# Kernel optimization log

Hardware: AMD Instinct MI355X
Metric: run time of the kernel (lower is better)

Reference implementation:

```python
import jax, jax.numpy as jnp
import numpy as np

T = 0.2
EPS = 1e-05


def setup_inputs() -> dict:
    key = jax.random.key(0)
    k1, k2 = jax.random.split(key)
    N, D, NUM_CLASSES = 8192, 128, 128
    inp = jax.random.normal(k1, (N, D), dtype=jnp.float32)
    label = jax.random.randint(k2, (N,), 0, NUM_CLASSES, dtype=jnp.int64)
    return {"input": inp, "label": label}


def reference(input, label):
    # Pairwise cosine similarity: dot(x_i, x_j) / max(||x_i|| * ||x_j||, eps)
    norms = jnp.sqrt(jnp.sum(input * input, axis=1))            # [N]
    denom = jnp.maximum(norms[:, None] * norms[None, :], EPS)   # [N, N]
    sim = (input @ input.T) / denom                             # [N, N]

    mask = (label[:, None] == label[None, :]).astype(input.dtype)  # same-label mask
    e = jnp.exp(sim / T)
    e = e - jnp.diag(jnp.diag(e))                               # zero the diagonal

    pos = mask * e                                              # positives (diag already 0)
    unsim = jnp.sum(e - pos, axis=-1, keepdims=True)            # [N, 1] negatives row-sum
    ratio = pos / (pos + unsim)                                 # per-pair NT-Xent prob
    safe = jnp.where(ratio > 0, ratio, 1.0)                     # loss[loss<=0] = 1
    loss_sum = jnp.sum(-jnp.log(safe))

    # number of off-diagonal positive pairs
    off_diag_mask = mask - jnp.diag(jnp.diag(mask))
    n_pos = jnp.count_nonzero(off_diag_mask).astype(input.dtype)
    return loss_sum / n_pos
```

## Files before the change

kernel.cpp:

```cpp
#include <hip/hip_runtime.h>
#include <math.h>

typedef float f32x4 __attribute__((ext_vector_type(4)));
typedef __attribute__((address_space(3))) unsigned int lds_u32;
typedef __attribute__((address_space(1))) const unsigned int glb_u32;

__global__ __launch_bounds__(256) void norm_kernel(
    const float* __restrict__ X, unsigned char* __restrict__ Y8,
    float inv_sqrtT) {
  int t = threadIdx.x;
  int row = blockIdx.x * 8 + (t >> 5);
  int l32 = t & 31;
  float4 v = ((const float4*)(X + (size_t)row * 128))[l32];
  float s = v.x * v.x + v.y * v.y + v.z * v.z + v.w * v.w;
  s += __shfl_xor(s, 1);
  s += __shfl_xor(s, 2);
  s += __shfl_xor(s, 4);
  s += __shfl_xor(s, 8);
  s += __shfl_xor(s, 16);
  float inv = inv_sqrtT * rsqrtf(fmaxf(s, 1e-24f));
  int pk = __builtin_amdgcn_cvt_pk_fp8_f32(v.x * inv, v.y * inv, 0, false);
  pk = __builtin_amdgcn_cvt_pk_fp8_f32(v.z * inv, v.w * inv, pk, true);
  int chunk = l32 >> 2;
  int off = ((chunk ^ (row & 7)) << 4) + ((l32 & 3) << 2);
  *(unsigned int*)(Y8 + (size_t)row * 128 + off) = (unsigned)pk;
}

__global__ __launch_bounds__(256, 2) void pass1_kernel(
    const unsigned char* __restrict__ Y8, const int* __restrict__ lab,
    float* __restrict__ P, float* __restrict__ Q, float* __restrict__ S,
    int N) {
  __shared__ unsigned char As[128][128];
  __shared__ unsigned char Bs[2][128][128];
  __shared__ int labR[128];
  __shared__ float tsumS[128], psumS[128], diagS[128];
  __shared__ float sS[4];

  const int b = blockIdx.x;
  const int bi = b >> 3, c = b & 7;
  const int i0 = bi * 128;
  const int t = threadIdx.x;
  const int w = t >> 6, lane = t & 63;

#pragma unroll
  for (int k = 0; k < 4; ++k) {
    const int c0 = w * 64 + k * 256;
    const int cc = c0 + lane;
    __builtin_amdgcn_global_load_lds(
        (glb_u32*)(Y8 + (size_t)i0 * 128 + (size_t)cc * 16),
        (lds_u32*)((unsigned char*)&As[0][0] + c0 * 16), 16, 0, 0);
    __builtin_amdgcn_global_load_lds(
        (glb_u32*)(Y8 + (size_t)(c * 8) * 128 * 128 + (size_t)cc * 16),
        (lds_u32*)((unsigned char*)&Bs[0][0][0] + c0 * 16), 16, 0, 0);
  }
  if (t < 128) {
    labR[t] = lab[i0 + t];
    psumS[t] = 0.f;
    diagS[t] = 0.f;
  }
  __syncthreads();

  const int quad = lane >> 4, l16 = lane & 15;
  const int rbase = w * 32;
  const int sw = l16 & 7;

  long af[4][2];
#pragma unroll
  for (int ks = 0; ks < 4; ++ks) {
    const int ch = ks * 2 + (quad >> 1);
    const int off = ((ch ^ sw) << 4) + ((quad & 1) << 3);
#pragma unroll
    for (int p = 0; p < 2; ++p)
      af[ks][p] = *(const long*)&As[rbase + p * 16 + l16][off];
  }
  int lr[2][4];
#pragma unroll
  for (int pi = 0; pi < 2; ++pi)
#pragma unroll
    for (int r = 0; r < 4; ++r)
      lr[pi][r] = labR[rbase + pi * 16 + quad * 4 + r];

  float trow[2][4] = {};
  float sacc = 0.f;

#pragma unroll 2
  for (int jt = 0; jt < 8; ++jt) {
    const int cur = jt & 1;
    const int jtile = c * 8 + jt;
    const int jt0 = jtile * 128;

    if (jt < 7) {
      const unsigned char* src = Y8 + (size_t)(jt0 + 128) * 128;
      unsigned char* dst = (unsigned char*)&Bs[cur ^ 1][0][0];
#pragma unroll
      for (int k = 0; k < 4; ++k) {
        const int c0 = w * 64 + k * 256;
        const int cc = c0 + lane;
        __builtin_amdgcn_global_load_lds((glb_u32*)(src + (size_t)cc * 16),
                                         (lds_u32*)(dst + c0 * 16), 16, 0, 0);
      }
    }

    int lc[8];
#pragma unroll
    for (int pj = 0; pj < 8; ++pj) lc[pj] = lab[jt0 + pj * 16 + l16];

    f32x4 acc[2][8] = {};
#pragma unroll
    for (int ks = 0; ks < 4; ++ks) {
      const int ch = ks * 2 + (quad >> 1);
      const int off = ((ch ^ sw) << 4) + ((quad & 1) << 3);
      long bf[8];
#pragma unroll
      for (int p = 0; p < 8; ++p)
        bf[p] = *(const long*)&Bs[cur][p * 16 + l16][off];
#pragma unroll
      for (int pi = 0; pi < 2; ++pi)
#pragma unroll
        for (int pj = 0; pj < 8; ++pj)
          acc[pi][pj] = __builtin_amdgcn_mfma_f32_16x16x32_fp8_fp8(
              af[ks][pi], bf[pj], acc[pi][pj], 0, 0, 0);
    }

    const bool dtile = (jtile == bi);
#pragma unroll
    for (int pi = 0; pi < 2; ++pi)
#pragma unroll
      for (int pj = 0; pj < 8; ++pj)
#pragma unroll
        for (int r = 0; r < 4; ++r) {
          const float s = acc[pi][pj][r];
          const float e = __expf(s);
          trow[pi][r] += e;
          if (lr[pi][r] == lc[pj]) {
            const int rowl = rbase + pi * 16 + quad * 4 + r;
            const int cl = pj * 16 + l16;
            if (dtile && rowl == cl) {
              diagS[rowl] = e;
            } else {
              atomicAdd(&psumS[rowl], e);
              sacc += s;
            }
          }
        }
    __syncthreads();
  }

#pragma unroll
  for (int pi = 0; pi < 2; ++pi)
#pragma unroll
    for (int r = 0; r < 4; ++r) {
      float v = trow[pi][r];
      v += __shfl_xor(v, 1);
      v += __shfl_xor(v, 2);
      v += __shfl_xor(v, 4);
      v += __shfl_xor(v, 8);
      if (l16 == 0) tsumS[rbase + pi * 16 + quad * 4 + r] = v;
    }
#pragma unroll
  for (int m = 1; m < 64; m <<= 1) sacc += __shfl_xor(sacc, m);
  if (lane == 0) sS[w] = sacc;
  __syncthreads();

  if (t < 128) {
    const int gi = i0 + t;
    P[c * N + gi] = tsumS[t] - diagS[t];
    Q[c * N + gi] = psumS[t];
  }
  if (t == 0) S[b] = sS[0] + sS[1] + sS[2] + sS[3];
}

__global__ __launch_bounds__(1024) void finalize_kernel(
    const int* __restrict__ lab, const float* __restrict__ P,
    const float* __restrict__ Q, const float* __restrict__ S,
    float* __restrict__ out, int N) {
  __shared__ int hist[256];
  __shared__ float redL[16], redN[16], redS[16];
  int t = threadIdx.x;
  int lane = t & 63, w = t >> 6;
  if (t < 256) hist[t] = 0;
  __syncthreads();
  for (int i = t; i < N; i += 1024) atomicAdd(&hist[lab[i] & 255], 1);
  __syncthreads();
  float local = 0.f;
  for (int i = t; i < N; i += 1024) {
    float tot = 0.f, p = 0.f;
#pragma unroll
    for (int cc = 0; cc < 8; ++cc) {
      tot += P[cc * N + i];
      p += Q[cc * N + i];
    }
    float u = tot - p;
    float cnt = (float)(hist[lab[i] & 255] - 1);
    local += cnt * __logf(u) + p / u;
  }
  float nposl = 0.f;
  if (t < 256) {
    float m = (float)hist[t];
    nposl = m * m;
  }
  float sl = (t < 512) ? S[t] : 0.f;
#pragma unroll
  for (int msk = 1; msk < 64; msk <<= 1) {
    local += __shfl_xor(local, msk);
    nposl += __shfl_xor(nposl, msk);
    sl += __shfl_xor(sl, msk);
  }
  if (lane == 0) {
    redL[w] = local;
    redN[w] = nposl;
    redS[w] = sl;
  }
  __syncthreads();
  if (t == 0) {
    float ls = 0.f, np = 0.f, ss = 0.f;
#pragma unroll
    for (int i = 0; i < 16; ++i) {
      ls += redL[i];
      np += redN[i];
      ss += redS[i];
    }
    out[0] = (ls - ss) / (np - (float)N);
  }
}

extern "C" void kernel_launch(void* const* d_in, const int* in_sizes, int n_in,
                              void* d_out, int out_size, void* d_ws,
                              size_t ws_size, hipStream_t stream) {
  const float* X = (const float*)d_in[0];
  const int* lab = (const int*)d_in[1];
  float* out = (float*)d_out;

  const int N = in_sizes[1];

  unsigned char* Y8 = (unsigned char*)d_ws;
  float* P = (float*)(Y8 + (size_t)N * 128);
  float* Q = P + 8 * (size_t)N;
  float* S = Q + 8 * (size_t)N;

  const float inv_sqrtT = 2.2360679775f;
  norm_kernel<<<N / 8, 256, 0, stream>>>(X, Y8, inv_sqrtT);

  const int nblk = (N / 128) * 8;
  pass1_kernel<<<nblk, 256, 0, stream>>>(Y8, lab, P, Q, S, N);
  finalize_kernel<<<1, 1024, 0, stream>>>(lab, P, Q, S, out, N);
}
```

Before: 98.47 us.

## Split column work finer, drop LDS atomics, parallelize finalize across blocks

The main pass now gives each block a 512-column slice, processed as eight 64-column tiles, with 16 column groups instead of 8. That doubles the grid and halves the B-tile LDS footprint so four blocks can share a CU. The per-row positive sums now accumulate in registers with branchless selects, replacing shared-memory atomics, and diagonal handling only happens in the phase that holds the diagonal. The finalize step is spread over N/256 blocks that atomically add into an output zeroed by the norm kernel. In exchange, A fragments are re-read from LDS every tile, the histogram is rebuilt in every finalize block, and the float atomic sum is no longer deterministic.

```diff
diff --git a/kernel.cpp b/kernel.cpp
--- a/kernel.cpp
+++ b/kernel.cpp
@@ -7,7 +7,7 @@
 
 __global__ __launch_bounds__(256) void norm_kernel(
     const float* __restrict__ X, unsigned char* __restrict__ Y8,
-    float inv_sqrtT) {
+    float* __restrict__ out, float inv_sqrtT) {
   int t = threadIdx.x;
   int row = blockIdx.x * 8 + (t >> 5);
   int l32 = t & 31;
@@ -24,21 +24,22 @@
   int chunk = l32 >> 2;
   int off = ((chunk ^ (row & 7)) << 4) + ((l32 & 3) << 2);
   *(unsigned int*)(Y8 + (size_t)row * 128 + off) = (unsigned)pk;
-}
-
-__global__ __launch_bounds__(256, 2) void pass1_kernel(
+  if (blockIdx.x == 0 && t == 0) out[0] = 0.f;
+}
+
+__global__ __launch_bounds__(256, 4) void pass1_kernel(
     const unsigned char* __restrict__ Y8, const int* __restrict__ lab,
     float* __restrict__ P, float* __restrict__ Q, float* __restrict__ S,
     int N) {
   __shared__ unsigned char As[128][128];
-  __shared__ unsigned char Bs[2][128][128];
+  __shared__ unsigned char Bs[2][64][128];
   __shared__ int labR[128];
-  __shared__ float tsumS[128], psumS[128], diagS[128];
   __shared__ float sS[4];
 
   const int b = blockIdx.x;
-  const int bi = b >> 3, c = b & 7;
+  const int bi = b >> 4, c = b & 15;
   const int i0 = bi * 128;
+  const int j0 = c * 512;
   const int t = threadIdx.x;
   const int w = t >> 6, lane = t & 63;
 
@@ -49,30 +50,22 @@
     __builtin_amdgcn_global_load_lds(
         (glb_u32*)(Y8 + (size_t)i0 * 128 + (size_t)cc * 16),
         (lds_u32*)((unsigned char*)&As[0][0] + c0 * 16), 16, 0, 0);
+  }
+#pragma unroll
+  for (int k = 0; k < 2; ++k) {
+    const int c0 = w * 64 + k * 256;
+    const int cc = c0 + lane;
     __builtin_amdgcn_global_load_lds(
-        (glb_u32*)(Y8 + (size_t)(c * 8) * 128 * 128 + (size_t)cc * 16),
+        (glb_u32*)(Y8 + (size_t)j0 * 128 + (size_t)cc * 16),
         (lds_u32*)((unsigned char*)&Bs[0][0][0] + c0 * 16), 16, 0, 0);
   }
-  if (t < 128) {
-    labR[t] = lab[i0 + t];
-    psumS[t] = 0.f;
-    diagS[t] = 0.f;
-  }
+  if (t < 128) labR[t] = lab[i0 + t];
   __syncthreads();
 
   const int quad = lane >> 4, l16 = lane & 15;
   const int rbase = w * 32;
   const int sw = l16 & 7;
 
-  long af[4][2];
-#pragma unroll
-  for (int ks = 0; ks < 4; ++ks) {
-    const int ch = ks * 2 + (quad >> 1);
-    const int off = ((ch ^ sw) << 4) + ((quad & 1) << 3);
-#pragma unroll
-    for (int p = 0; p < 2; ++p)
-      af[ks][p] = *(const long*)&As[rbase + p * 16 + l16][off];
-  }
   int lr[2][4];
 #pragma unroll
   for (int pi = 0; pi < 2; ++pi)
@@ -81,19 +74,18 @@
       lr[pi][r] = labR[rbase + pi * 16 + quad * 4 + r];
 
   float trow[2][4] = {};
+  float pr[2][4] = {};
   float sacc = 0.f;
 
-#pragma unroll 2
   for (int jt = 0; jt < 8; ++jt) {
     const int cur = jt & 1;
-    const int jtile = c * 8 + jt;
-    const int jt0 = jtile * 128;
+    const int jt0 = j0 + jt * 64;
 
     if (jt < 7) {
-      const unsigned char* src = Y8 + (size_t)(jt0 + 128) * 128;
+      const unsigned char* src = Y8 + (size_t)(jt0 + 64) * 128;
       unsigned char* dst = (unsigned char*)&Bs[cur ^ 1][0][0];
 #pragma unroll
-      for (int k = 0; k < 4; ++k) {
+      for (int k = 0; k < 2; ++k) {
         const int c0 = w * 64 + k * 256;
         const int cc = c0 + lane;
         __builtin_amdgcn_global_load_lds((glb_u32*)(src + (size_t)cc * 16),
@@ -101,48 +93,65 @@
       }
     }
 
-    int lc[8];
-#pragma unroll
-    for (int pj = 0; pj < 8; ++pj) lc[pj] = lab[jt0 + pj * 16 + l16];
-
-    f32x4 acc[2][8] = {};
+    int lc[4], cg[4];
+#pragma unroll
+    for (int pj = 0; pj < 4; ++pj) {
+      cg[pj] = jt0 + pj * 16 + l16;
+      lc[pj] = lab[cg[pj]];
+    }
+
+    f32x4 acc[2][4] = {};
 #pragma unroll
     for (int ks = 0; ks < 4; ++ks) {
       const int ch = ks * 2 + (quad >> 1);
       const int off = ((ch ^ sw) << 4) + ((quad & 1) << 3);
-      long bf[8];
-#pragma unroll
-      for (int p = 0; p < 8; ++p)
+      long af[2], bf[4];
+#pragma unroll
+      for (int p = 0; p < 2; ++p)
+        af[p] = *(const long*)&As[rbase + p * 16 + l16][off];
+#pragma unroll
+      for (int p = 0; p < 4; ++p)
         bf[p] = *(const long*)&Bs[cur][p * 16 + l16][off];
 #pragma unroll
       for (int pi = 0; pi < 2; ++pi)
 #pragma unroll
-        for (int pj = 0; pj < 8; ++pj)
+        for (int pj = 0; pj < 4; ++pj)
           acc[pi][pj] = __builtin_amdgcn_mfma_f32_16x16x32_fp8_fp8(
-              af[ks][pi], bf[pj], acc[pi][pj], 0, 0, 0);
-    }
-
-    const bool dtile = (jtile == bi);
-#pragma unroll
-    for (int pi = 0; pi < 2; ++pi)
-#pragma unroll
-      for (int pj = 0; pj < 8; ++pj)
-#pragma unroll
-        for (int r = 0; r < 4; ++r) {
-          const float s = acc[pi][pj][r];
-          const float e = __expf(s);
-          trow[pi][r] += e;
-          if (lr[pi][r] == lc[pj]) {
+              af[pi], bf[pj], acc[pi][pj], 0, 0, 0);
+    }
+
+    const bool dphase = ((jt0 >> 7) == bi);
+    if (dphase) {
+#pragma unroll
+      for (int pi = 0; pi < 2; ++pi)
+#pragma unroll
+        for (int pj = 0; pj < 4; ++pj)
+#pragma unroll
+          for (int r = 0; r < 4; ++r) {
+            const float s = acc[pi][pj][r];
+            const float e = __expf(s);
             const int rowl = rbase + pi * 16 + quad * 4 + r;
-            const int cl = pj * 16 + l16;
-            if (dtile && rowl == cl) {
-              diagS[rowl] = e;
-            } else {
-              atomicAdd(&psumS[rowl], e);
-              sacc += s;
-            }
+            const bool self = (i0 + rowl) == cg[pj];
+            const bool match = (lr[pi][r] == lc[pj]) && !self;
+            trow[pi][r] += self ? 0.f : e;
+            pr[pi][r] += match ? e : 0.f;
+            sacc += match ? s : 0.f;
           }
-        }
+    } else {
+#pragma unroll
+      for (int pi = 0; pi < 2; ++pi)
+#pragma unroll
+        for (int pj = 0; pj < 4; ++pj)
+#pragma unroll
+          for (int r = 0; r < 4; ++r) {
+            const float s = acc[pi][pj][r];
+            const float e = __expf(s);
+            const bool match = (lr[pi][r] == lc[pj]);
+            trow[pi][r] += e;
+            pr[pi][r] += match ? e : 0.f;
+            sacc += match ? s : 0.f;
+          }
+    }
     __syncthreads();
   }
 
@@ -150,77 +159,63 @@
   for (int pi = 0; pi < 2; ++pi)
 #pragma unroll
     for (int r = 0; r < 4; ++r) {
-      float v = trow[pi][r];
+      float v = trow[pi][r], q = pr[pi][r];
       v += __shfl_xor(v, 1);
+      q += __shfl_xor(q, 1);
       v += __shfl_xor(v, 2);
+      q += __shfl_xor(q, 2);
       v += __shfl_xor(v, 4);
+      q += __shfl_xor(q, 4);
       v += __shfl_xor(v, 8);
-      if (l16 == 0) tsumS[rbase + pi * 16 + quad * 4 + r] = v;
+      q += __shfl_xor(q, 8);
+      if (l16 == 0) {
+        const int row = rbase + pi * 16 + quad * 4 + r;
+        P[c * N + i0 + row] = v;
+        Q[c * N + i0 + row] = q;
+      }
     }
 #pragma unroll
   for (int m = 1; m < 64; m <<= 1) sacc += __shfl_xor(sacc, m);
   if (lane == 0) sS[w] = sacc;
   __syncthreads();
-
-  if (t < 128) {
-    const int gi = i0 + t;
-    P[c * N + gi] = tsumS[t] - diagS[t];
-    Q[c * N + gi] = psumS[t];
-  }
   if (t == 0) S[b] = sS[0] + sS[1] + sS[2] + sS[3];
 }
 
-__global__ __launch_bounds__(1024) void finalize_kernel(
+__global__ __launch_bounds__(256) void finalize_kernel(
     const int* __restrict__ lab, const float* __restrict__ P,
     const float* __restrict__ Q, const float* __restrict__ S,
     float* __restrict__ out, int N) {
   __shared__ int hist[256];
-  __shared__ float redL[16], redN[16], redS[16];
-  int t = threadIdx.x;
-  int lane = t & 63, w = t >> 6;
-  if (t < 256) hist[t] = 0;
-  __syncthreads();
-  for (int i = t; i < N; i += 1024) atomicAdd(&hist[lab[i] & 255], 1);
-  __syncthreads();
-  float local = 0.f;
-  for (int i = t; i < N; i += 1024) {
-    float tot = 0.f, p = 0.f;
-#pragma unroll
-    for (int cc = 0; cc < 8; ++cc) {
-      tot += P[cc * N + i];
-      p += Q[cc * N + i];
-    }
-    float u = tot - p;
-    float cnt = (float)(hist[lab[i] & 255] - 1);
-    local += cnt * __logf(u) + p / u;
-  }
-  float nposl = 0.f;
-  if (t < 256) {
-    float m = (float)hist[t];
-    nposl = m * m;
-  }
-  float sl = (t < 512) ? S[t] : 0.f;
-#pragma unroll
-  for (int msk = 1; msk < 64; msk <<= 1) {
-    local += __shfl_xor(local, msk);
-    nposl += __shfl_xor(nposl, msk);
-    sl += __shfl_xor(sl, msk);
-  }
-  if (lane == 0) {
-    redL[w] = local;
-    redN[w] = nposl;
-    redS[w] = sl;
-  }
+  __shared__ float red[4];
+  const int b = blockIdx.x, t = threadIdx.x;
+  const int lane = t & 63, w = t >> 6;
+  hist[t] = 0;
+  __syncthreads();
+  for (int i = t; i < N; i += 256) atomicAdd(&hist[lab[i] & 255], 1);
+  __syncthreads();
+
+  const int i = b * 256 + t;
+  float tot = 0.f, p = 0.f;
+#pragma unroll
+  for (int cc = 0; cc < 16; ++cc) {
+    tot += P[cc * N + i];
+    p += Q[cc * N + i];
+  }
+  const float u = tot - p;
+  const float cnti = (float)(hist[lab[i] & 255] - 1);
+  float local = cnti * __logf(u) + p / u;
+  if (t < 32) local -= S[b * 32 + t];
+#pragma unroll
+  for (int m = 1; m < 64; m <<= 1) local += __shfl_xor(local, m);
+  if (lane == 0) red[w] = local;
   __syncthreads();
   if (t == 0) {
-    float ls = 0.f, np = 0.f, ss = 0.f;
-#pragma unroll
-    for (int i = 0; i < 16; ++i) {
-      ls += redL[i];
-      np += redN[i];
-      ss += redS[i];
-    }
-    out[0] = (ls - ss) / (np - (float)N);
+    float np = 0.f;
+    for (int k = 0; k < 256; ++k) {
+      const float m = (float)hist[k];
+      np += m * m;
+    }
+    atomicAdd(out, (red[0] + red[1] + red[2] + red[3]) / (np - (float)N));
   }
 }
 
@@ -235,13 +230,13 @@
 
   unsigned char* Y8 = (unsigned char*)d_ws;
   float* P = (float*)(Y8 + (size_t)N * 128);
-  float* Q = P + 8 * (size_t)N;
-  float* S = Q + 8 * (size_t)N;
+  float* Q = P + 16 * (size_t)N;
+  float* S = Q + 16 * (size_t)N;
 
   const float inv_sqrtT = 2.2360679775f;
-  norm_kernel<<<N / 8, 256, 0, stream>>>(X, Y8, inv_sqrtT);
-
-  const int nblk = (N / 128) * 8;
+  norm_kernel<<<N / 8, 256, 0, stream>>>(X, Y8, out, inv_sqrtT);
+
+  const int nblk = (N / 128) * 16;
   pass1_kernel<<<nblk, 256, 0, stream>>>(Y8, lab, P, Q, S, N);
-  finalize_kernel<<<1, 1024, 0, stream>>>(lab, P, Q, S, out, N);
-}
+  finalize_kernel<<<N / 256, 256, 0, stream>>>(lab, P, Q, S, out, N);
+}
```

Result: no change. 98.40 us (-0.1%).
